# Performance work log

Measured on AMD Instinct MI355X. Metric: run time of the kernel, lower is better.

Reference implementation:

```python
import jax, jax.numpy as jnp
import numpy as np

B, S, H, NH = 8, 1024, 768, 12
I = 3072
HD = H // NH  # 64


def setup_inputs() -> dict:
    key = jax.random.key(0)
    ks = jax.random.split(key, 6)
    w = lambda k, shape: jax.random.normal(k, shape, jnp.float32) * 0.02
    return {
        "x": jax.random.normal(ks[0], (B, S, H), jnp.float32),
        "ln1_g": jnp.ones((H,), jnp.float32),
        "ln1_b": jnp.zeros((H,), jnp.float32),
        "qkv_w": w(ks[1], (H, 3 * H)),
        "qkv_b": jnp.zeros((3 * H,), jnp.float32),
        "proj_w": w(ks[2], (H, H)),
        "proj_b": jnp.zeros((H,), jnp.float32),
        "ln2_g": jnp.ones((H,), jnp.float32),
        "ln2_b": jnp.zeros((H,), jnp.float32),
        "fc1_w": w(ks[3], (H, I)),
        "fc1_b": jnp.zeros((I,), jnp.float32),
        "fc2_w": w(ks[4], (I, H)),
        "fc2_b": jnp.zeros((H,), jnp.float32),
    }


def _layernorm(x, g, b, eps=1e-5):
    m = x.mean(-1, keepdims=True)
    v = x.var(-1, keepdims=True)  # biased variance, matches torch LayerNorm
    return (x - m) * jax.lax.rsqrt(v + eps) * g + b


def _new_gelu(x):
    c = np.float32(np.sqrt(2.0 / np.pi))
    return 0.5 * x * (1.0 + jnp.tanh(c * (x + 0.044715 * x * x * x)))


def reference(x, ln1_g, ln1_b, qkv_w, qkv_b, proj_w, proj_b,
              ln2_g, ln2_b, fc1_w, fc1_b, fc2_w, fc2_b):
    # --- attention sublayer (pre-LN) ---
    h = _layernorm(x, ln1_g, ln1_b)                     # [B,S,H]
    qkv = h @ qkv_w + qkv_b                             # [B,S,3H]
    q, k, v = jnp.split(qkv, 3, axis=-1)
    q = q.reshape(B, S, NH, HD).transpose(0, 2, 1, 3)   # [B,NH,S,HD]
    k = k.reshape(B, S, NH, HD).transpose(0, 2, 1, 3)
    v = v.reshape(B, S, NH, HD).transpose(0, 2, 1, 3)
    scores = jnp.einsum('bhtd,bhsd->bhts', q, k) / np.float32(np.sqrt(HD))
    probs = jax.nn.softmax(scores, axis=-1)             # [B,NH,S,S]
    attn = jnp.einsum('bhts,bhsd->bhtd', probs, v)      # [B,NH,S,HD]
    attn = attn.transpose(0, 2, 1, 3).reshape(B, S, H)
    attn = attn @ proj_w + proj_b
    x = x + attn
    # --- MLP sublayer (pre-LN) ---
    h2 = _layernorm(x, ln2_g, ln2_b)
    m = _new_gelu(h2 @ fc1_w + fc1_b) @ fc2_w + fc2_b
    return x + m
```

## Files before the change

kernel.cpp:

```cpp
#include <hip/hip_runtime.h>
#include <hip/hip_bf16.h>


typedef __attribute__((ext_vector_type(8))) short bf16x8;
typedef __attribute__((ext_vector_type(4))) float f32x4;
typedef const __attribute__((address_space(3))) char* lds_cp;

#define MFMA16(a, b, c) __builtin_amdgcn_mfma_f32_16x16x32_bf16((a), (b), (c), 0, 0, 0)

#define DSR(dst, addr, off) \
    asm volatile("ds_read_b128 %0, %1 offset:" #off : "=v"(dst) : "v"(addr))
#define WAITV4 asm volatile("s_waitcnt vmcnt(4)" ::: "memory")
#define WAITV0 asm volatile("s_waitcnt vmcnt(0)" ::: "memory")
#define WAITLG asm volatile("s_waitcnt lgkmcnt(0)" ::: "memory")
#define SCHEDB __builtin_amdgcn_sched_barrier(0)

__device__ inline short f2bf(float x) {
    __hip_bfloat16 h = __float2bfloat16(x);
    return *reinterpret_cast<short*>(&h);
}

__device__ inline void gload_lds16(const void* g, void* lds) {
    __builtin_amdgcn_global_load_lds(
        (const __attribute__((address_space(1))) unsigned int*)g,
        (__attribute__((address_space(3))) unsigned int*)lds,
        16, 0, 0);
}

__global__ __launch_bounds__(256) void transpose_w(
    const float* __restrict__ W, short* __restrict__ Wt, int K, int N) {
    __shared__ float tile[32][33];
    const int tx = threadIdx.x & 31, ty = threadIdx.x >> 5;
    const int n0 = blockIdx.x * 32, k0 = blockIdx.y * 32;
#pragma unroll
    for (int i = 0; i < 4; ++i)
        tile[ty + i * 8][tx] = W[(size_t)(k0 + ty + i * 8) * N + n0 + tx];
    __syncthreads();
#pragma unroll
    for (int i = 0; i < 4; ++i)
        Wt[(size_t)(n0 + ty + i * 8) * K + k0 + tx] = f2bf(tile[tx][ty + i * 8]);
}

__global__ __launch_bounds__(256) void ln_k(
    const float* __restrict__ x, const float* __restrict__ g,
    const float* __restrict__ b, short* __restrict__ out) {
    const int row = blockIdx.x;
    const int tid = threadIdx.x;
    const float* xr = x + (size_t)row * 768;
    float v[3];
    float s = 0.f, sq = 0.f;
#pragma unroll
    for (int i = 0; i < 3; ++i) {
        v[i] = xr[tid + i * 256];
        s += v[i];
        sq += v[i] * v[i];
    }
#pragma unroll
    for (int off = 32; off >= 1; off >>= 1) {
        s += __shfl_xor(s, off);
        sq += __shfl_xor(sq, off);
    }
    __shared__ float ss[4], ssq[4];
    const int wid = tid >> 6;
    if ((tid & 63) == 0) { ss[wid] = s; ssq[wid] = sq; }
    __syncthreads();
    s = ss[0] + ss[1] + ss[2] + ss[3];
    sq = ssq[0] + ssq[1] + ssq[2] + ssq[3];
    const float mean = s * (1.0f / 768.0f);
    const float var = sq * (1.0f / 768.0f) - mean * mean;
    const float rstd = rsqrtf(var + 1e-5f);
    short* outr = out + (size_t)row * 768;
#pragma unroll
    for (int i = 0; i < 3; ++i) {
        const int c = tid + i * 256;
        outr[c] = f2bf((v[i] - mean) * rstd * g[c] + b[c]);
    }
}

enum { MODE_BF16 = 0, MODE_QKV = 1, MODE_F32RES = 2, MODE_GELU = 3 };

template <int MODE>
__global__ __launch_bounds__(256) void gemm3p(
    const short* __restrict__ A, const short* __restrict__ Wt,
    const float* __restrict__ bias, const float* __restrict__ resid,
    float* __restrict__ outf, short* __restrict__ outh,
    short* __restrict__ Qo, short* __restrict__ Ko, short* __restrict__ Vto,
    int M, int N, int K) {
    __shared__ __attribute__((aligned(128))) short Al[3][4096];
    __shared__ __attribute__((aligned(128))) short Bl[3][4096];
    const int tid = threadIdx.x;
    const int lane = tid & 63;
    const int w = tid >> 6;
    const int wm = w >> 1, wn = w & 1;
    const int m0 = blockIdx.x * 128, n0 = blockIdx.y * 128;

    f32x4 acc[4][4] = {};

    const int srow = tid >> 2;
    const int scol = ((tid & 3) * 8) ^ (((tid >> 2) & 3) << 3);
    const short* Abase = A + (size_t)(m0 + srow) * K + scol;
    const short* Bbase = Wt + (size_t)(n0 + srow) * K + scol;
    const size_t K64 = (size_t)K * 64;
    short* const AlF = &Al[0][0];
    short* const BlF = &Bl[0][0];

    auto stageT = [&](int boS, int k0s) {
        gload_lds16(Abase + k0s,       AlF + boS + w * 512);
        gload_lds16(Abase + K64 + k0s, AlF + boS + 2048 + w * 512);
        gload_lds16(Bbase + k0s,       BlF + boS + w * 512);
        gload_lds16(Bbase + K64 + k0s, BlF + boS + 2048 + w * 512);
    };

    const int lrow = lane & 15;
    const int lcolswz = ((lane >> 4) * 16) ^ ((lane & 3) << 4);
    const int aoff = wm * 4096 + lrow * 64 + lcolswz;
    const int boff = wn * 4096 + lrow * 64 + lcolswz;
    const lds_cp AlB = (lds_cp)AlF;
    const lds_cp BlB = (lds_cp)BlF;

    const int NT = K >> 5;

    stageT(0, 0);
    stageT(4096, 32);
    WAITV4;
    SCHEDB;
    __builtin_amdgcn_s_barrier();

    int bo = 0, bo1 = 8192, bo2 = 16384;
    for (int t = 0; t < NT; ++t) {
        const lds_cp Ab = AlB + (bo + aoff);
        const lds_cp Bb = BlB + (bo + boff);
        bf16x8 av0, av1, av2, av3, bv0, bv1, bv2, bv3;
        DSR(av0, Ab, 0);
        DSR(av1, Ab, 1024);
        DSR(av2, Ab, 2048);
        DSR(av3, Ab, 3072);
        DSR(bv0, Bb, 0);
        DSR(bv1, Bb, 1024);
        DSR(bv2, Bb, 2048);
        DSR(bv3, Bb, 3072);

        int ts = t + 2;
        if (ts > NT - 1) ts = NT - 1;
        stageT(bo2 >> 1, ts << 5);
        WAITV4;
        SCHEDB;
        __builtin_amdgcn_s_barrier();
        WAITLG;
        SCHEDB;

        __builtin_amdgcn_s_setprio(1);
        {
            bf16x8 av[4] = {av0, av1, av2, av3};
            bf16x8 bv[4] = {bv0, bv1, bv2, bv3};
#pragma unroll
            for (int mi = 0; mi < 4; ++mi)
#pragma unroll
                for (int ni = 0; ni < 4; ++ni)
                    acc[mi][ni] = MFMA16(av[mi], bv[ni], acc[mi][ni]);
        }
        __builtin_amdgcn_s_setprio(0);
        __builtin_amdgcn_s_barrier();

        const int tmp = bo; bo = bo1; bo1 = bo2; bo2 = tmp;
    }
    WAITV0;

#pragma unroll
    for (int mi = 0; mi < 4; ++mi) {
#pragma unroll
        for (int ni = 0; ni < 4; ++ni) {
#pragma unroll
            for (int r = 0; r < 4; ++r) {
                const int row = m0 + wm * 64 + mi * 16 + (lane >> 4) * 4 + r;
                const int col = n0 + wn * 64 + ni * 16 + (lane & 15);
                float v = acc[mi][ni][r] + bias[col];
                if constexpr (MODE == MODE_BF16) {
                    outh[(size_t)row * N + col] = f2bf(v);
                } else if constexpr (MODE == MODE_GELU) {
                    const float u = 0.7978845608028654f * (v + 0.044715f * v * v * v);
                    const float gl = v / (1.0f + __expf(-2.0f * u));
                    outh[(size_t)row * N + col] = f2bf(gl);
                } else if constexpr (MODE == MODE_F32RES) {
                    outf[(size_t)row * N + col] = v + resid[(size_t)row * N + col];
                } else {
                    const int bb = row >> 10, s = row & 1023;
                    if (col < 768) {
                        const int hh = col >> 6, d = col & 63;
                        Qo[(((size_t)(bb * 12 + hh)) * 1024 + s) * 64 + d] = f2bf(v);
                    } else if (col < 1536) {
                        const int c2 = col - 768;
                        const int hh = c2 >> 6, d = c2 & 63;
                        Ko[(((size_t)(bb * 12 + hh)) * 1024 + s) * 64 + d] = f2bf(v);
                    } else {
                        const int c2 = col - 1536;
                        const int hh = c2 >> 6, d = c2 & 63;
                        Vto[(((size_t)(bb * 12 + hh)) * 64 + d) * 1024 + s] = f2bf(v);
                    }
                }
            }
        }
    }
}

__global__ __launch_bounds__(256) void attn_k(
    const short* __restrict__ Q, const short* __restrict__ Kg,
    const short* __restrict__ Vtg, short* __restrict__ out) {
    __shared__ __attribute__((aligned(128))) short Kl[64 * 64];
    __shared__ __attribute__((aligned(128))) short Vl[64 * 64];
    __shared__ __attribute__((aligned(128))) short Pl[4][16 * 64];
    const int tid = threadIdx.x, lane = tid & 63, w = tid >> 6;
    const int swz = (blockIdx.x & 7) * 192 + (blockIdx.x >> 3);
    const int qt = swz & 15, bh = swz >> 4;
    const int b = bh / 12, h = bh % 12;
    const int q0 = qt * 64 + w * 16;

    const int l15 = lane & 15, g = lane >> 4;

    bf16x8 aq[2];
    const short* Qb = Q + ((size_t)bh * 1024 + q0) * 64;
#pragma unroll
    for (int kk = 0; kk < 2; ++kk)
        aq[kk] = *(const bf16x8*)&Qb[(size_t)l15 * 64 + kk * 32 + g * 8];

    float m_run[4], l_run[4];
    f32x4 o[4] = {};
#pragma unroll
    for (int r = 0; r < 4; ++r) { m_run[r] = -1e30f; l_run[r] = 0.f; }

    const short* Kb = Kg + (size_t)bh * 1024 * 64;
    const short* Vb = Vtg + (size_t)bh * 64 * 1024;

    for (int kv0 = 0; kv0 < 1024; kv0 += 64) {
        for (int c = tid; c < 512; c += 256) {
            const int rr = c >> 3, pp = (c & 7) * 8;
            const int sc = pp ^ ((rr & 7) << 3);
            *(bf16x8*)&Kl[rr * 64 + sc] = *(const bf16x8*)&Kb[(size_t)(kv0 + rr) * 64 + pp];
            *(bf16x8*)&Vl[rr * 64 + sc] = *(const bf16x8*)&Vb[(size_t)rr * 1024 + kv0 + pp];
        }
        __syncthreads();

        f32x4 sc4[4];
#pragma unroll
        for (int nk = 0; nk < 4; ++nk) {
            const int R = nk * 16 + l15;
            const int x = (R & 7) << 3;
            const bf16x8 kb0 = *(const bf16x8*)&Kl[R * 64 + ((g * 8) ^ x)];
            const bf16x8 kb1 = *(const bf16x8*)&Kl[R * 64 + ((32 + g * 8) ^ x)];
            f32x4 z = {};
            z = MFMA16(aq[0], kb0, z);
            z = MFMA16(aq[1], kb1, z);
            sc4[nk] = z * 0.125f;
        }

        float alpha[4], padd[4][4];
#pragma unroll
        for (int r = 0; r < 4; ++r) {
            float ml = fmaxf(fmaxf(sc4[0][r], sc4[1][r]), fmaxf(sc4[2][r], sc4[3][r]));
#pragma unroll
            for (int mk = 1; mk <= 8; mk <<= 1) ml = fmaxf(ml, __shfl_xor(ml, mk));
            const float mn = fmaxf(m_run[r], ml);
            alpha[r] = __expf(m_run[r] - mn);
            m_run[r] = mn;
            float rsum = 0.f;
#pragma unroll
            for (int nk = 0; nk < 4; ++nk) {
                padd[nk][r] = __expf(sc4[nk][r] - mn);
                rsum += padd[nk][r];
            }
#pragma unroll
            for (int mk = 1; mk <= 8; mk <<= 1) rsum += __shfl_xor(rsum, mk);
            l_run[r] = l_run[r] * alpha[r] + rsum;
#pragma unroll
            for (int dn = 0; dn < 4; ++dn) o[dn][r] *= alpha[r];
        }

#pragma unroll
        for (int nk = 0; nk < 4; ++nk)
#pragma unroll
            for (int r = 0; r < 4; ++r) {
                const int rr = g * 4 + r, cc = nk * 16 + l15;
                Pl[w][rr * 64 + (cc ^ ((rr & 7) << 3))] = f2bf(padd[nk][r]);
            }
        bf16x8 pa[2];
#pragma unroll
        for (int kk = 0; kk < 2; ++kk)
            pa[kk] = *(const bf16x8*)&Pl[w][l15 * 64 + ((kk * 32 + g * 8) ^ ((l15 & 7) << 3))];

#pragma unroll
        for (int dn = 0; dn < 4; ++dn) {
            const int R = dn * 16 + l15;
            const int x = (R & 7) << 3;
            const bf16x8 bv0 = *(const bf16x8*)&Vl[R * 64 + ((g * 8) ^ x)];
            const bf16x8 bv1 = *(const bf16x8*)&Vl[R * 64 + ((32 + g * 8) ^ x)];
            o[dn] = MFMA16(pa[0], bv0, o[dn]);
            o[dn] = MFMA16(pa[1], bv1, o[dn]);
        }
        __syncthreads();
    }

#pragma unroll
    for (int dn = 0; dn < 4; ++dn)
#pragma unroll
        for (int r = 0; r < 4; ++r) {
            const int srow = q0 + g * 4 + r;
            const float v = o[dn][r] / l_run[r];
            out[((size_t)(b * 1024) + srow) * 768 + h * 64 + dn * 16 + l15] = f2bf(v);
        }
}

extern "C" void kernel_launch(void* const* d_in, const int* in_sizes, int n_in,
                              void* d_out, int out_size, void* d_ws, size_t ws_size,
                              hipStream_t stream) {
    const float* x      = (const float*)d_in[0];
    const float* ln1_g  = (const float*)d_in[1];
    const float* ln1_b  = (const float*)d_in[2];
    const float* qkv_w  = (const float*)d_in[3];
    const float* qkv_b  = (const float*)d_in[4];
    const float* proj_w = (const float*)d_in[5];
    const float* proj_b = (const float*)d_in[6];
    const float* ln2_g  = (const float*)d_in[7];
    const float* ln2_b  = (const float*)d_in[8];
    const float* fc1_w  = (const float*)d_in[9];
    const float* fc1_b  = (const float*)d_in[10];
    const float* fc2_w  = (const float*)d_in[11];
    const float* fc2_b  = (const float*)d_in[12];
    float* outp = (float*)d_out;

    char* ws = (char*)d_ws;
    size_t off = 0;
    auto alloc = [&](size_t bytes) {
        char* p = ws + off;
        off = (off + bytes + 255) & ~(size_t)255;
        return p;
    };
    short* wt_qkv  = (short*)alloc(2304ull * 768 * 2);
    short* wt_proj = (short*)alloc(768ull * 768 * 2);
    short* wt_fc1  = (short*)alloc(3072ull * 768 * 2);
    short* wt_fc2  = (short*)alloc(768ull * 3072 * 2);
    short* hbuf    = (short*)alloc(8192ull * 768 * 2);
    short* Qb      = (short*)alloc(8192ull * 768 * 2);
    short* Kbuf    = (short*)alloc(8192ull * 768 * 2);
    short* Vtb     = (short*)alloc(8192ull * 768 * 2);
    short* attnb   = (short*)alloc(8192ull * 768 * 2);
    float* x2      = (float*)alloc(8192ull * 768 * 4);
    short* mfc     = Qb;
    (void)ws_size; (void)in_sizes; (void)n_in; (void)out_size;

    transpose_w<<<dim3(2304 / 32, 768 / 32), 256, 0, stream>>>(qkv_w, wt_qkv, 768, 2304);
    transpose_w<<<dim3(768 / 32, 768 / 32), 256, 0, stream>>>(proj_w, wt_proj, 768, 768);
    transpose_w<<<dim3(3072 / 32, 768 / 32), 256, 0, stream>>>(fc1_w, wt_fc1, 768, 3072);
    transpose_w<<<dim3(768 / 32, 3072 / 32), 256, 0, stream>>>(fc2_w, wt_fc2, 3072, 768);

    ln_k<<<8192, 256, 0, stream>>>(x, ln1_g, ln1_b, hbuf);
    gemm3p<MODE_QKV><<<dim3(64, 18), 256, 0, stream>>>(
        hbuf, wt_qkv, qkv_b, nullptr, nullptr, nullptr, Qb, Kbuf, Vtb, 8192, 2304, 768);
    attn_k<<<1536, 256, 0, stream>>>(Qb, Kbuf, Vtb, attnb);
    gemm3p<MODE_F32RES><<<dim3(64, 6), 256, 0, stream>>>(
        attnb, wt_proj, proj_b, x, x2, nullptr, nullptr, nullptr, nullptr, 8192, 768, 768);

    ln_k<<<8192, 256, 0, stream>>>(x2, ln2_g, ln2_b, hbuf);
    gemm3p<MODE_GELU><<<dim3(64, 24), 256, 0, stream>>>(
        hbuf, wt_fc1, fc1_b, nullptr, nullptr, mfc, nullptr, nullptr, nullptr, 8192, 3072, 768);
    gemm3p<MODE_F32RES><<<dim3(64, 6), 256, 0, stream>>>(
        mfc, wt_fc2, fc2_b, x2, outp, nullptr, nullptr, nullptr, nullptr, 8192, 768, 3072);
}
```

Measured before the change: 310.4 us.

## Double-buffer attention K/V tiles with async global-to-LDS loads

The attention kernel now keeps two LDS buffers for K and V and issues global_load_lds for the next tile while the current tile is computed, replacing the synchronous register-staged copy. K/V fragment reads use explicit ds_read_b128 with a single wait before the MFMAs. The 1/sqrt(d) scale is folded into Q in the QKV epilogue, and the final normalization uses a reciprocal multiply instead of a division. This doubles K/V LDS usage and relies on the wait/barrier placement being correct for the async copies.

```diff
diff --git a/kernel.cpp b/kernel.cpp
--- a/kernel.cpp
+++ b/kernel.cpp
@@ -187,7 +187,7 @@
                     const int bb = row >> 10, s = row & 1023;
                     if (col < 768) {
                         const int hh = col >> 6, d = col & 63;
-                        Qo[(((size_t)(bb * 12 + hh)) * 1024 + s) * 64 + d] = f2bf(v);
+                        Qo[(((size_t)(bb * 12 + hh)) * 1024 + s) * 64 + d] = f2bf(v * 0.125f);
                     } else if (col < 1536) {
                         const int c2 = col - 768;
                         const int hh = c2 >> 6, d = c2 & 63;
@@ -206,15 +206,14 @@
 __global__ __launch_bounds__(256) void attn_k(
     const short* __restrict__ Q, const short* __restrict__ Kg,
     const short* __restrict__ Vtg, short* __restrict__ out) {
-    __shared__ __attribute__((aligned(128))) short Kl[64 * 64];
-    __shared__ __attribute__((aligned(128))) short Vl[64 * 64];
+    __shared__ __attribute__((aligned(128))) short Kl[2][64 * 64];
+    __shared__ __attribute__((aligned(128))) short Vl[2][64 * 64];
     __shared__ __attribute__((aligned(128))) short Pl[4][16 * 64];
     const int tid = threadIdx.x, lane = tid & 63, w = tid >> 6;
     const int swz = (blockIdx.x & 7) * 192 + (blockIdx.x >> 3);
     const int qt = swz & 15, bh = swz >> 4;
     const int b = bh / 12, h = bh % 12;
     const int q0 = qt * 64 + w * 16;
-
     const int l15 = lane & 15, g = lane >> 4;
 
     bf16x8 aq[2];
@@ -231,26 +230,47 @@
     const short* Kb = Kg + (size_t)bh * 1024 * 64;
     const short* Vb = Vtg + (size_t)bh * 64 * 1024;
 
-    for (int kv0 = 0; kv0 < 1024; kv0 += 64) {
-        for (int c = tid; c < 512; c += 256) {
-            const int rr = c >> 3, pp = (c & 7) * 8;
-            const int sc = pp ^ ((rr & 7) << 3);
-            *(bf16x8*)&Kl[rr * 64 + sc] = *(const bf16x8*)&Kb[(size_t)(kv0 + rr) * 64 + pp];
-            *(bf16x8*)&Vl[rr * 64 + sc] = *(const bf16x8*)&Vb[(size_t)rr * 1024 + kv0 + pp];
-        }
-        __syncthreads();
-
-        f32x4 sc4[4];
+    const int srr = tid >> 3;
+    const int spp = (tid & 7) * 8;
+    const int ssc = spp ^ ((srr & 7) << 3);
+    auto stage = [&](int buf, int kv0) {
+        gload_lds16(Kb + (size_t)(kv0 + srr) * 64 + ssc,      &Kl[buf][w * 512]);
+        gload_lds16(Kb + (size_t)(kv0 + 32 + srr) * 64 + ssc, &Kl[buf][2048 + w * 512]);
+        gload_lds16(Vb + (size_t)srr * 1024 + kv0 + ssc,      &Vl[buf][w * 512]);
+        gload_lds16(Vb + (size_t)(srr + 32) * 1024 + kv0 + ssc, &Vl[buf][2048 + w * 512]);
+    };
+
+    stage(0, 0);
+    __syncthreads();
+
+    int buf = 0;
+    for (int t = 0; t < 16; ++t) {
+        const lds_cp KB = (lds_cp)&Kl[buf][0];
+        const lds_cp VB = (lds_cp)&Vl[buf][0];
+
+        bf16x8 kb[4][2];
 #pragma unroll
         for (int nk = 0; nk < 4; ++nk) {
             const int R = nk * 16 + l15;
-            const int x = (R & 7) << 3;
-            const bf16x8 kb0 = *(const bf16x8*)&Kl[R * 64 + ((g * 8) ^ x)];
-            const bf16x8 kb1 = *(const bf16x8*)&Kl[R * 64 + ((32 + g * 8) ^ x)];
+            const int c0 = (g * 8) ^ ((R & 7) << 3);
+            const lds_cp a0 = KB + R * 128 + c0 * 2;
+            const lds_cp a1 = KB + R * 128 + (c0 ^ 32) * 2;
+            DSR(kb[nk][0], a0, 0);
+            DSR(kb[nk][1], a1, 0);
+        }
+
+        if (t < 15) stage(buf ^ 1, (t + 1) * 64);
+
+        WAITLG;
+        SCHEDB;
+
+        f32x4 sc4[4];
+#pragma unroll
+        for (int nk = 0; nk < 4; ++nk) {
             f32x4 z = {};
-            z = MFMA16(aq[0], kb0, z);
-            z = MFMA16(aq[1], kb1, z);
-            sc4[nk] = z * 0.125f;
+            z = MFMA16(aq[0], kb[nk][0], z);
+            z = MFMA16(aq[1], kb[nk][1], z);
+            sc4[nk] = z;
         }
 
         float alpha[4], padd[4][4];
@@ -287,26 +307,38 @@
         for (int kk = 0; kk < 2; ++kk)
             pa[kk] = *(const bf16x8*)&Pl[w][l15 * 64 + ((kk * 32 + g * 8) ^ ((l15 & 7) << 3))];
 
+        bf16x8 vb[4][2];
 #pragma unroll
         for (int dn = 0; dn < 4; ++dn) {
             const int R = dn * 16 + l15;
-            const int x = (R & 7) << 3;
-            const bf16x8 bv0 = *(const bf16x8*)&Vl[R * 64 + ((g * 8) ^ x)];
-            const bf16x8 bv1 = *(const bf16x8*)&Vl[R * 64 + ((32 + g * 8) ^ x)];
-            o[dn] = MFMA16(pa[0], bv0, o[dn]);
-            o[dn] = MFMA16(pa[1], bv1, o[dn]);
-        }
+            const int c0 = (g * 8) ^ ((R & 7) << 3);
+            const lds_cp a0 = VB + R * 128 + c0 * 2;
+            const lds_cp a1 = VB + R * 128 + (c0 ^ 32) * 2;
+            DSR(vb[dn][0], a0, 0);
+            DSR(vb[dn][1], a1, 0);
+        }
+        WAITLG;
+        SCHEDB;
+
+#pragma unroll
+        for (int dn = 0; dn < 4; ++dn) {
+            o[dn] = MFMA16(pa[0], vb[dn][0], o[dn]);
+            o[dn] = MFMA16(pa[1], vb[dn][1], o[dn]);
+        }
+
         __syncthreads();
-    }
-
-#pragma unroll
-    for (int dn = 0; dn < 4; ++dn)
-#pragma unroll
-        for (int r = 0; r < 4; ++r) {
-            const int srow = q0 + g * 4 + r;
-            const float v = o[dn][r] / l_run[r];
-            out[((size_t)(b * 1024) + srow) * 768 + h * 64 + dn * 16 + l15] = f2bf(v);
-        }
+        buf ^= 1;
+    }
+
+#pragma unroll
+    for (int r = 0; r < 4; ++r) {
+        const float rl = __builtin_amdgcn_rcpf(l_run[r]);
+        const int srow = q0 + g * 4 + r;
+#pragma unroll
+        for (int dn = 0; dn < 4; ++dn)
+            out[((size_t)(b * 1024) + srow) * 768 + h * 64 + dn * 16 + l15] =
+                f2bf(o[dn][r] * rl);
+    }
 }
 
 extern "C" void kernel_launch(void* const* d_in, const int* in_sizes, int n_in,
```

Result: no change. 308.6 us (-0.6%).
